# Kernel tuning notes

Measured on AMD Instinct MI355X. Metric: run time of the kernel, lower is better.

The kernel has to match this reference:

```python
import jax, jax.numpy as jnp
import numpy as np

H, D, K = 8, 64, 9           # new num heads, head size, conv kernel size
A = H * D                    # all_head_size = 512
HID = 2 * A                  # input hidden size = 1024
STD = 0.02


def setup_inputs() -> dict:
    key = jax.random.key(0)
    ks = jax.random.split(key, 16)
    B, S = 4, 2048
    f = jnp.float32
    inp = {
        'hidden_states': jax.random.normal(ks[0], (B, S, HID), f),
        'Wq': jax.random.normal(ks[1], (A, A), f) * STD,
        'bq': jnp.zeros((A,), f),
        'Wk': jax.random.normal(ks[2], (A, A), f) * STD,
        'bk': jnp.zeros((A,), f),
        'Wv': jax.random.normal(ks[3], (A, A), f) * STD,
        'bv': jnp.zeros((A,), f),
        'dw_w': jax.random.normal(ks[4], (A, 1, K), f) * STD,   # depthwise conv (groups=A)
        'pw_w': jax.random.normal(ks[5], (A, A, 1), f) * STD,   # pointwise 1x1 conv
        'sep_b': jnp.zeros((A, 1), f),                          # SeparableConv1D bias
        'Wck': jax.random.normal(ks[6], (H * K, A), f) * STD,   # conv_kernel_layer
        'bck': jnp.zeros((H * K,), f),
        'Wco': jax.random.normal(ks[7], (A, A), f) * STD,       # conv_out_layer
        'bco': jnp.zeros((A,), f),
    }
    return inp


def reference(hidden_states, Wq, bq, Wk, bk, Wv, bv, dw_w, pw_w, sep_b, Wck, bck, Wco, bco):
    B, S, _ = hidden_states.shape
    hs_attn = hidden_states[:, :, :A]
    hs_conv = hidden_states[:, :, A:]

    q = hs_attn @ Wq.T + bq
    k = hs_attn @ Wk.T + bk
    v = hs_attn @ Wv.T + bv

    # SeparableConv1D on (B, A, S): depthwise then pointwise, plus bias
    x = hs_conv.transpose(0, 2, 1)
    x = jax.lax.conv_general_dilated(
        x, dw_w, window_strides=(1,), padding=[(K // 2, K // 2)],
        feature_group_count=A, dimension_numbers=('NCH', 'OIH', 'NCH'))
    x = jnp.einsum('bcs,oc->bos', x, pw_w[:, :, 0]) + sep_b
    mixed_key_conv = x.transpose(0, 2, 1)            # (B,S,A)

    # per-token softmax conv kernel
    conv_attn = mixed_key_conv * hs_conv
    ckl = (conv_attn @ Wck.T + bck).reshape(B, S, H, K)
    ckl = jax.nn.softmax(ckl, axis=-1)               # softmax over kernel taps

    # dynamic-span lightweight convolution (unfold -> batched matmul)
    col = hs_conv @ Wco.T + bco                      # (B,S,A)
    pad = jnp.pad(col, ((0, 0), (K // 2, K // 2), (0, 0)))
    windows = jnp.stack([pad[:, i:i + S] for i in range(K)], axis=-1)  # (B,S,A,K)
    windows = windows.reshape(B, S, H, D, K)
    conv_out = jnp.einsum('bshdk,bshk->bshd', windows, ckl)            # (B,S,H,D)

    # standard self-attention
    qh = q.reshape(B, S, H, D).transpose(0, 2, 1, 3)
    kh = k.reshape(B, S, H, D).transpose(0, 2, 1, 3)
    vh = v.reshape(B, S, H, D).transpose(0, 2, 1, 3)
    scale = jnp.asarray(1.0 / np.sqrt(D), q.dtype)
    scores = jnp.einsum('bhqd,bhkd->bhqk', qh, kh) * scale
    probs = jax.nn.softmax(scores, axis=-1)
    ctx = jnp.einsum('bhqk,bhkd->bqhd', probs, vh)   # (B,S,H,D)

    out = jnp.concatenate([ctx, conv_out], axis=2)   # (B,S,2H,D)
    return out.reshape(B, S, HID)
```

## Files before the change

### kernel.cpp

```cpp
#include <hip/hip_runtime.h>
#include <hip/hip_bf16.h>

#define NH   8
#define HD   64
#define KW   9
#define AD   512
#define HIDD 1024
#define BB   4
#define SS   2048
#define MTOK (BB*SS)
#define WSZ  262144

typedef __attribute__((ext_vector_type(8))) short short8;
typedef __attribute__((ext_vector_type(4))) float floatx4;
typedef __attribute__((ext_vector_type(16))) float floatx16;

__device__ __forceinline__ short f2bf(float f) {
    unsigned u = __float_as_uint(f);
    u = (u + 0x7FFFu + ((u >> 16) & 1u)) >> 16;
    return (short)u;
}
__device__ __forceinline__ float bf2f(short s) {
    return __uint_as_float(((unsigned)(unsigned short)s) << 16);
}
__device__ __forceinline__ float exp2_raw(float x) {
    return __builtin_amdgcn_exp2f(x);
}
__device__ __forceinline__ unsigned pkbf2(float a, float b) {
    unsigned d;
    asm("v_cvt_pk_bf16_f32 %0, %1, %2" : "=v"(d) : "v"(a), "v"(b));
    return d;
}
__device__ __forceinline__ void gl2lds16(const short* g, short* l) {
    __builtin_amdgcn_global_load_lds(
        (const __attribute__((address_space(1))) void*)g,
        (__attribute__((address_space(3))) void*)l, 16, 0, 0);
}

__global__ __launch_bounds__(256) void cvt_hs_kernel(
    const float* __restrict__ hs, short* __restrict__ hsb)
{
    int idx = blockIdx.x * 256 + threadIdx.x;
    const float* s = hs + (long)idx * 8;
    float4 a = *(const float4*)s, c = *(const float4*)(s + 4);
    short8 o;
    o[0]=f2bf(a.x); o[1]=f2bf(a.y); o[2]=f2bf(a.z); o[3]=f2bf(a.w);
    o[4]=f2bf(c.x); o[5]=f2bf(c.y); o[6]=f2bf(c.z); o[7]=f2bf(c.w);
    *(short8*)(hsb + (long)idx * 8) = o;
}

__global__ __launch_bounds__(256) void cvt_w_kernel(
    const float* __restrict__ pw, const float* __restrict__ Wco,
    const float* __restrict__ Wq, const float* __restrict__ Wk,
    const float* __restrict__ Wv, const float* __restrict__ Wck,
    const float* __restrict__ dw,
    short* __restrict__ dst, float* __restrict__ dwT)
{
    int idx = blockIdx.x * 256 + threadIdx.x;
    if (idx >= 172032) {
        int t = idx - 172032;
        if (t < AD * KW) {
            int c = t / KW, k = t - c * KW;
            dwT[k * AD + c] = dw[t];
        }
        return;
    }
    int e0 = idx * 8;
    short8 o;
    if (e0 < 5 * WSZ) {
        int w = e0 >> 18, off = e0 & (WSZ - 1);
        const float* src = (w == 0) ? pw : (w == 1) ? Wco : (w == 2) ? Wq
                         : (w == 3) ? Wk : Wv;
        float4 a = *(const float4*)(src + off), c = *(const float4*)(src + off + 4);
        o[0]=f2bf(a.x); o[1]=f2bf(a.y); o[2]=f2bf(a.z); o[3]=f2bf(a.w);
        o[4]=f2bf(c.x); o[5]=f2bf(c.y); o[6]=f2bf(c.z); o[7]=f2bf(c.w);
    } else {
        int off = e0 - 5 * WSZ;
        int row = off >> 9, col = off & 511;
        if (row < NH * KW) {
            const float* src = Wck + row * AD + col;
            float4 a = *(const float4*)src, c = *(const float4*)(src + 4);
            o[0]=f2bf(a.x); o[1]=f2bf(a.y); o[2]=f2bf(a.z); o[3]=f2bf(a.w);
            o[4]=f2bf(c.x); o[5]=f2bf(c.y); o[6]=f2bf(c.z); o[7]=f2bf(c.w);
        } else {
            for (int i = 0; i < 8; ++i) o[i] = 0;
        }
    }
    *(short8*)(dst + e0) = o;
}

__global__ __launch_bounds__(256) void dwconv_kernel(
    const short* __restrict__ hsb, const float* __restrict__ dwT,
    short* __restrict__ x1)
{
    int idx = blockIdx.x * 256 + threadIdx.x;
    int c8  = (idx & 63) * 8;
    int tok = idx >> 6;
    int s   = tok & (SS - 1);
    int b   = tok >> 11;
    const short* base = hsb + (long)(b * SS) * HIDD + AD + c8;
    float acc[8];
#pragma unroll
    for (int i = 0; i < 8; ++i) acc[i] = 0.f;
#pragma unroll
    for (int kk = 0; kk < KW; ++kk) {
        int ss2 = s + kk - KW / 2;
        if (ss2 >= 0 && ss2 < SS) {
            short8 hv = *(const short8*)(base + (long)ss2 * HIDD);
            float4 w0 = *(const float4*)(dwT + kk * AD + c8);
            float4 w1 = *(const float4*)(dwT + kk * AD + c8 + 4);
            acc[0] += w0.x * bf2f(hv[0]); acc[1] += w0.y * bf2f(hv[1]);
            acc[2] += w0.z * bf2f(hv[2]); acc[3] += w0.w * bf2f(hv[3]);
            acc[4] += w1.x * bf2f(hv[4]); acc[5] += w1.y * bf2f(hv[5]);
            acc[6] += w1.z * bf2f(hv[6]); acc[7] += w1.w * bf2f(hv[7]);
        }
    }
    short8 o;
#pragma unroll
    for (int i = 0; i < 8; ++i) o[i] = f2bf(acc[i]);
    *(short8*)(x1 + (long)tok * AD + c8) = o;
}

template<int FM, int FN, int MODE>
__global__ __launch_bounds__(256) void gemm_bf16_kernel(
    const short* __restrict__ X, int ldx, int xoff,
    const short* __restrict__ W,
    const float* __restrict__ b0p, const float* __restrict__ b1p,
    const float* __restrict__ b2p,
    const short* __restrict__ mulp, int mul_ld, int mul_off,
    void* __restrict__ Cout, short* __restrict__ vtout,
    int ldc, int N, int Kd, float oscale)
{
    constexpr int TM = 32 * FM, TN = 32 * FN;
    __shared__ __align__(16) short As[TM * 64];
    __shared__ __align__(16) short Bs[TN * 64];
    const int tid  = threadIdx.x;
    const int wv   = tid >> 6, lane = tid & 63;
    const int ln   = lane & 15, quad = lane >> 4;
    const int wm   = wv >> 1, wn = wv & 1;
    const int m0 = blockIdx.x * TM, n0 = blockIdx.y * TN;

    floatx4 acc[FM][FN];
#pragma unroll
    for (int i = 0; i < FM; ++i)
#pragma unroll
        for (int j = 0; j < FN; ++j) acc[i][j] = (floatx4){0.f, 0.f, 0.f, 0.f};

    const short* xbase = X + (long)m0 * ldx + xoff;
    const short* wbase = W + (long)n0 * Kd;

    for (int k0 = 0; k0 < Kd; k0 += 64) {
#pragma unroll
        for (int g = tid; g < TM * 8; g += 256) {
            int m = g >> 3, p = g & 7, gk = p ^ (m & 7);
            gl2lds16(xbase + (long)m * ldx + k0 + gk * 8, &As[g * 8]);
        }
#pragma unroll
        for (int g = tid; g < TN * 8; g += 256) {
            int m = g >> 3, p = g & 7, gk = p ^ (m & 7);
            gl2lds16(wbase + (long)m * Kd + k0 + gk * 8, &Bs[g * 8]);
        }
        __syncthreads();
#pragma unroll
        for (int half = 0; half < 2; ++half) {
            short8 afr[FM], bfr[FN];
#pragma unroll
            for (int i = 0; i < FM; ++i) {
                int p = (half * 4 + quad) ^ (ln & 7);
                afr[i] = *(const short8*)&As[(wm * 16 * FM + i * 16 + ln) * 64 + p * 8];
            }
#pragma unroll
            for (int j = 0; j < FN; ++j) {
                int p = (half * 4 + quad) ^ (ln & 7);
                bfr[j] = *(const short8*)&Bs[(wn * 16 * FN + j * 16 + ln) * 64 + p * 8];
            }
#pragma unroll
            for (int i = 0; i < FM; ++i)
#pragma unroll
                for (int j = 0; j < FN; ++j)
                    acc[i][j] = __builtin_amdgcn_mfma_f32_16x16x32_bf16(
                        afr[i], bfr[j], acc[i][j], 0, 0, 0);
        }
        __syncthreads();
    }

#pragma unroll
    for (int j = 0; j < FN; ++j) {
        int n = n0 + wn * 16 * FN + j * 16 + ln;
        if constexpr (MODE == 3) {
            if (n >= 1024) {
                int hh = (n - 1024) >> 6, dd = (n - 1024) & 63;
                float bv = b2p[n - 1024];
                int mblk = m0 + wm * 16 * FM;
                int bidx = mblk >> 11, sblk = mblk & (SS - 1);
                short* dst = vtout + ((long)((bidx * NH + hh) * HD + dd)) * SS + sblk;
#pragma unroll
                for (int i = 0; i < FM; ++i) {
                    unsigned lo = pkbf2(acc[i][j][0] + bv, acc[i][j][1] + bv);
                    unsigned hi = pkbf2(acc[i][j][2] + bv, acc[i][j][3] + bv);
                    *(uint2*)(dst + i * 16 + quad * 4) = make_uint2(lo, hi);
                }
            } else {
                float bv = (n < 512) ? b0p[n] : b1p[n - 512];
                float sc = (n < 512) ? oscale : 1.f;
#pragma unroll
                for (int i = 0; i < FM; ++i) {
#pragma unroll
                    for (int r = 0; r < 4; ++r) {
                        int m = m0 + wm * 16 * FM + i * 16 + quad * 4 + r;
                        float val = (acc[i][j][r] + bv) * sc;
                        ((short*)Cout)[(long)m * ldc + n] = f2bf(val);
                    }
                }
            }
        } else if (n < N) {
            float bv = b0p[n], sc = oscale;
#pragma unroll
            for (int i = 0; i < FM; ++i) {
#pragma unroll
                for (int r = 0; r < 4; ++r) {
                    int m = m0 + wm * 16 * FM + i * 16 + quad * 4 + r;
                    float val = (acc[i][j][r] + bv) * sc;
                    if constexpr (MODE == 2)
                        val *= bf2f(mulp[(long)m * mul_ld + mul_off + n]);
                    if constexpr (MODE == 0)
                        ((float*)Cout)[(long)m * ldc + n] = val;
                    else
                        ((short*)Cout)[(long)m * ldc + n] = f2bf(val);
                }
            }
        }
    }
}

__global__ __launch_bounds__(256) void convout_kernel(
    const short* __restrict__ col, const float* __restrict__ ckl,
    float* __restrict__ out)
{
    int idx = blockIdx.x * 256 + threadIdx.x;
    int d4  = (idx & 127) * 4;
    int tok = idx >> 7;
    int s   = tok & (SS - 1);
    int b   = tok >> 11;
    int h   = d4 >> 6;
    const float* lg = ckl + (long)tok * (NH * KW) + h * KW;
    float wv[KW];
    float mx = -1e30f;
#pragma unroll
    for (int i = 0; i < KW; ++i) { wv[i] = lg[i]; mx = fmaxf(mx, wv[i]); }
    float sum = 0.f;
#pragma unroll
    for (int i = 0; i < KW; ++i) { wv[i] = __expf(wv[i] - mx); sum += wv[i]; }
    float inv = 1.f / sum;
    float a0 = 0.f, a1 = 0.f, a2 = 0.f, a3 = 0.f;
    const short* cbase = col + (long)(b * SS) * AD + d4;
#pragma unroll
    for (int kk = 0; kk < KW; ++kk) {
        int ss2 = s + kk - KW / 2;
        if (ss2 >= 0 && ss2 < SS) {
            uint2 cv = *(const uint2*)(cbase + (long)ss2 * AD);
            float w = wv[kk];
            a0 += w * bf2f((short)(cv.x & 0xFFFF));
            a1 += w * bf2f((short)(cv.x >> 16));
            a2 += w * bf2f((short)(cv.y & 0xFFFF));
            a3 += w * bf2f((short)(cv.y >> 16));
        }
    }
    *(float4*)&out[(long)tok * HIDD + AD + d4] =
        make_float4(a0 * inv, a1 * inv, a2 * inv, a3 * inv);
}

__global__ __launch_bounds__(256) void flash_mfma_kernel(
    const short* __restrict__ qkv, const short* __restrict__ vT,
    float* __restrict__ out)
{
    const int qt = blockIdx.x, h = blockIdx.y, b = blockIdx.z;
    const int tid  = threadIdx.x;
    const int w    = tid >> 6;
    const int lane = tid & 63;
    const int l5   = lane & 31;
    const int hh   = lane >> 5;

    __shared__ __align__(16) short Kb[3][4096];
    __shared__ __align__(16) short Vb[3][4096];
    __shared__ float ls[4][32];

    const int  q0 = qt * 128 + w * 32;
    const long rowbase = (long)b * SS;

    short8 qf[4];
    {
        const short* qrow = qkv + (rowbase + q0 + l5) * 1536 + h * HD;
#pragma unroll
        for (int i = 0; i < 4; ++i)
            qf[i] = *(const short8*)(qrow + i * 16 + hh * 8);
    }

    floatx16 acc0, acc1;
    floatx16 Z;
#pragma unroll
    for (int r = 0; r < 16; ++r) { acc0[r] = 0.f; acc1[r] = 0.f; Z[r] = 0.f; }
    float l_i = 0.f;

    const int m1 = tid >> 3,  gk1 = (tid & 7) ^ (m1 & 7);
    const int g2 = 256 + tid;
    const int m2 = g2 >> 3,   gk2 = (g2 & 7) ^ (m2 & 7);
    const short* kbase  = qkv + 512 + rowbase * 1536 + h * HD;
    const short* vtbase = vT + ((long)(b * NH + h) * HD) * SS;
    const short* sk0 = kbase  + (long)m1 * 1536 + gk1 * 8;
    const short* sk1 = kbase  + (long)m2 * 1536 + gk2 * 8;
    const short* sv0 = vtbase + (long)m1 * SS   + gk1 * 8;
    const short* sv1 = vtbase + (long)m2 * SS   + gk2 * 8;

    auto STAGE_K = [&](int slot, bool adv) {
        gl2lds16(sk0, &Kb[slot][tid * 8]);
        gl2lds16(sk1, &Kb[slot][g2 * 8]);
        if (adv) { sk0 += 64 * 1536; sk1 += 64 * 1536; }
    };
    auto STAGE_V = [&](int slot) {
        gl2lds16(sv0, &Vb[slot][tid * 8]);
        gl2lds16(sv1, &Vb[slot][g2 * 8]);
        sv0 += 64; sv1 += 64;
    };

    auto qkt = [&](const short* KB, floatx16& S0, floatx16& S1) {
        {
            int p = hh ^ (l5 & 7);
            short8 k0 = *(const short8*)&KB[l5 * 64 + p * 8];
            short8 k1 = *(const short8*)&KB[(32 + l5) * 64 + p * 8];
            S0 = __builtin_amdgcn_mfma_f32_32x32x16_bf16(k0, qf[0], Z, 0, 0, 0);
            S1 = __builtin_amdgcn_mfma_f32_32x32x16_bf16(k1, qf[0], Z, 0, 0, 0);
        }
#pragma unroll
        for (int i = 1; i < 4; ++i) {
            int p = (2 * i + hh) ^ (l5 & 7);
            short8 k0 = *(const short8*)&KB[l5 * 64 + p * 8];
            short8 k1 = *(const short8*)&KB[(32 + l5) * 64 + p * 8];
            S0 = __builtin_amdgcn_mfma_f32_32x32x16_bf16(k0, qf[i], S0, 0, 0, 0);
            S1 = __builtin_amdgcn_mfma_f32_32x32x16_bf16(k1, qf[i], S1, 0, 0, 0);
        }
    };

    auto smax = [&](const floatx16& S0, const floatx16& S1, short8* pf) {
        float pe0[16], pe1[16];
#pragma unroll
        for (int r = 0; r < 16; ++r) {
            pe0[r] = exp2_raw(S0[r]);
            pe1[r] = exp2_raw(S1[r]);
        }
        float s = 0.f;
#pragma unroll
        for (int r = 0; r < 16; ++r) s += pe0[r] + pe1[r];
        l_i += s;
#pragma unroll
        for (int t = 0; t < 2; ++t) {
            const float* pe = t ? pe1 : pe0;
#pragma unroll
            for (int u = 0; u < 2; ++u) {
                unsigned a0 = pkbf2(pe[8 * u + 0], pe[8 * u + 1]);
                unsigned a1 = pkbf2(pe[8 * u + 2], pe[8 * u + 3]);
                unsigned b0 = pkbf2(pe[8 * u + 4], pe[8 * u + 5]);
                unsigned b1 = pkbf2(pe[8 * u + 6], pe[8 * u + 7]);
                asm("v_permlane32_swap_b32 %0, %1" : "+v"(a0), "+v"(b0));
                asm("v_permlane32_swap_b32 %0, %1" : "+v"(a1), "+v"(b1));
                union { uint4 u4; short8 s8; } cv;
                cv.u4 = make_uint4(a0, a1, b0, b1);
                pf[t * 2 + u] = cv.s8;
            }
        }
    };

    auto pv = [&](const short* VB, const short8* pf) {
#pragma unroll
        for (int s = 0; s < 4; ++s) {
            int p = (2 * s + hh) ^ (l5 & 7);
            short8 v0 = *(const short8*)&VB[l5 * 64 + p * 8];
            short8 v1 = *(const short8*)&VB[(32 + l5) * 64 + p * 8];
            acc0 = __builtin_amdgcn_mfma_f32_32x32x16_bf16(pf[s], v0, acc0, 0, 0, 0);
            acc1 = __builtin_amdgcn_mfma_f32_32x32x16_bf16(pf[s], v1, acc1, 0, 0, 0);
        }
    };

    short8 pfA[4], pfB[4];

    STAGE_K(0, true);
    STAGE_K(1, true);
    STAGE_V(0);
    asm volatile("s_waitcnt vmcnt(0)" ::: "memory");
    __builtin_amdgcn_s_barrier();
    asm volatile("" ::: "memory");

    {
        STAGE_K(2, true);
        STAGE_V(1);
        floatx16 S0, S1;
        qkt(Kb[0], S0, S1);
        smax(S0, S1, pfA);
        asm volatile("s_waitcnt vmcnt(4)" ::: "memory");
        __builtin_amdgcn_s_barrier();
        asm volatile("" ::: "memory");
    }

#define PHASE(KS, VPS, KST, VST, KADV, PIN, POUT)                      \
    {                                                                  \
        STAGE_K(KST, KADV);                                            \
        STAGE_V(VST);                                                  \
        floatx16 S0, S1;                                               \
        __builtin_amdgcn_s_setprio(1);                                 \
        qkt(Kb[KS], S0, S1);                                           \
        pv(Vb[VPS], PIN);                                              \
        __builtin_amdgcn_s_setprio(0);                                 \
        smax(S0, S1, POUT);                                            \
        asm volatile("s_waitcnt vmcnt(4)" ::: "memory");               \
        __builtin_amdgcn_s_barrier();                                  \
        asm volatile("" ::: "memory");                                 \
    }

    for (int g = 0; g < 5; ++g) {
        bool notlast = (g < 4);
        PHASE(1, 0, 0, 2, true,    pfA, pfB);
        PHASE(2, 1, 1, 0, true,    pfB, pfA);
        PHASE(0, 2, 2, 1, true,    pfA, pfB);
        PHASE(1, 0, 0, 2, true,    pfB, pfA);
        PHASE(2, 1, 1, 0, notlast, pfA, pfB);
        PHASE(0, 2, 2, 1, notlast, pfB, pfA);
    }
#undef PHASE

    {
        floatx16 S0, S1;
        __builtin_amdgcn_s_setprio(1);
        qkt(Kb[1], S0, S1);
        pv(Vb[0], pfA);
        __builtin_amdgcn_s_setprio(0);
        smax(S0, S1, pfB);
        asm volatile("s_waitcnt vmcnt(0)" ::: "memory");
        __builtin_amdgcn_s_barrier();
        asm volatile("" ::: "memory");
    }
    pv(Vb[1], pfB);

    l_i += __shfl_xor(l_i, 32);
    ls[w][l5] = 1.f / l_i;
    float4 lv[4];
#pragma unroll
    for (int g = 0; g < 4; ++g)
        lv[g] = *(const float4*)&ls[w][8 * g + 4 * hh];

#pragma unroll
    for (int r = 0; r < 16; ++r) {
        int g = r >> 2, j = r & 3;
        int qr = j + 8 * g + 4 * hh;
        float iv = lv[g][j];
        float* orow = out + (rowbase + q0 + qr) * HIDD + h * HD;
        orow[l5]      = acc0[r] * iv;
        orow[32 + l5] = acc1[r] * iv;
    }
}

extern "C" void kernel_launch(void* const* d_in, const int* in_sizes, int n_in,
                              void* d_out, int out_size, void* d_ws, size_t ws_size,
                              hipStream_t stream)
{
    const float* hs   = (const float*)d_in[0];
    const float* Wq   = (const float*)d_in[1];
    const float* bq   = (const float*)d_in[2];
    const float* Wk   = (const float*)d_in[3];
    const float* bk   = (const float*)d_in[4];
    const float* Wv   = (const float*)d_in[5];
    const float* bv   = (const float*)d_in[6];
    const float* dw   = (const float*)d_in[7];
    const float* pw   = (const float*)d_in[8];
    const float* sepb = (const float*)d_in[9];
    const float* Wck  = (const float*)d_in[10];
    const float* bck  = (const float*)d_in[11];
    const float* Wco  = (const float*)d_in[12];
    const float* bco  = (const float*)d_in[13];
    float* out = (float*)d_out;

    short* hsb  = (short*)d_ws;
    short* x1c  = hsb + (long)MTOK * HIDD;
    short* qkvb = x1c + (long)MTOK * AD;
    short* vTb  = qkvb + (long)MTOK * 1536;
    float* ckl  = (float*)(vTb + (long)MTOK * AD);
    short* wb   = (short*)(ckl + (long)MTOK * (NH * KW));
    short* pw_b   = wb;
    short* Wco_b  = wb + 1L * WSZ;
    short* Wqkv_b = wb + 2L * WSZ;
    short* Wck_b  = wb + 5L * WSZ;
    float* dwT    = (float*)(Wck_b + 128L * AD);
    short* cab    = qkvb;

    const float QSCALE = 0.18033688011112042f;

    cvt_hs_kernel<<<MTOK * HIDD / 2048, 256, 0, stream>>>(hs, hsb);
    cvt_w_kernel<<<690, 256, 0, stream>>>(
        pw, Wco, Wq, Wk, Wv, Wck, dw, wb, dwT);
    dwconv_kernel<<<MTOK * AD / 2048, 256, 0, stream>>>(hsb, dwT, x1c);
    gemm_bf16_kernel<2, 2, 2><<<dim3(MTOK / 64, AD / 64), 256, 0, stream>>>(
        x1c, AD, 0, pw_b, sepb, nullptr, nullptr, hsb, HIDD, AD,
        cab, nullptr, AD, AD, AD, 1.f);
    gemm_bf16_kernel<2, 2, 0><<<dim3(MTOK / 64, 2), 256, 0, stream>>>(
        cab, AD, 0, Wck_b, bck, nullptr, nullptr, nullptr, 0, 0,
        ckl, nullptr, NH * KW, NH * KW, AD, 1.f);
    gemm_bf16_kernel<2, 2, 1><<<dim3(MTOK / 64, AD / 64), 256, 0, stream>>>(
        hsb, HIDD, AD, Wco_b, bco, nullptr, nullptr, nullptr, 0, 0,
        x1c, nullptr, AD, AD, AD, 1.f);
    convout_kernel<<<MTOK * AD / 1024, 256, 0, stream>>>(x1c, ckl, out);
    gemm_bf16_kernel<4, 4, 3><<<dim3(MTOK / 128, 1536 / 128), 256, 0, stream>>>(
        hsb, HIDD, 0, Wqkv_b, bq, bk, bv, nullptr, 0, 0,
        qkvb, vTb, 1536, 1536, AD, QSCALE);
    flash_mfma_kernel<<<dim3(SS / 128, NH, BB), 256, 0, stream>>>(qkvb, vTb, out);

    (void)in_sizes; (void)n_in; (void)out_size; (void)ws_size;
}
```

Before: 220.1 us.

## Merge prep and independent GEMMs into fewer horizontally fused launches

Combines the hidden-state conversion, weight conversion and depthwise conv into one prep kernel. The depthwise conv now reads fp32 input directly and keeps its weights in LDS, so it no longer waits on the bf16 copy. The QKV GEMM and the pointwise GEMM now share one launch, and the Wco and Wck GEMMs share a second, using larger tiles. This is meant to cut launch overhead and fill the GPU better. The conv-attention intermediate is now staged in the output buffer, which relies on convout and flash overwriting it later. Every prep block also allocates 18KB of LDS, which may limit occupancy for the simple convert blocks.

```diff
diff --git a/kernel.cpp b/kernel.cpp
--- a/kernel.cpp
+++ b/kernel.cpp
@@ -37,92 +37,89 @@
         (__attribute__((address_space(3))) void*)l, 16, 0, 0);
 }
 
-__global__ __launch_bounds__(256) void cvt_hs_kernel(
-    const float* __restrict__ hs, short* __restrict__ hsb)
-{
-    int idx = blockIdx.x * 256 + threadIdx.x;
-    const float* s = hs + (long)idx * 8;
-    float4 a = *(const float4*)s, c = *(const float4*)(s + 4);
-    short8 o;
-    o[0]=f2bf(a.x); o[1]=f2bf(a.y); o[2]=f2bf(a.z); o[3]=f2bf(a.w);
-    o[4]=f2bf(c.x); o[5]=f2bf(c.y); o[6]=f2bf(c.z); o[7]=f2bf(c.w);
-    *(short8*)(hsb + (long)idx * 8) = o;
-}
-
-__global__ __launch_bounds__(256) void cvt_w_kernel(
+__global__ __launch_bounds__(256) void prep_kernel(
+    const float* __restrict__ hs,
     const float* __restrict__ pw, const float* __restrict__ Wco,
     const float* __restrict__ Wq, const float* __restrict__ Wk,
     const float* __restrict__ Wv, const float* __restrict__ Wck,
     const float* __restrict__ dw,
-    short* __restrict__ dst, float* __restrict__ dwT)
-{
-    int idx = blockIdx.x * 256 + threadIdx.x;
-    if (idx >= 172032) {
-        int t = idx - 172032;
-        if (t < AD * KW) {
-            int c = t / KW, k = t - c * KW;
-            dwT[k * AD + c] = dw[t];
-        }
-        return;
-    }
-    int e0 = idx * 8;
-    short8 o;
-    if (e0 < 5 * WSZ) {
-        int w = e0 >> 18, off = e0 & (WSZ - 1);
-        const float* src = (w == 0) ? pw : (w == 1) ? Wco : (w == 2) ? Wq
-                         : (w == 3) ? Wk : Wv;
-        float4 a = *(const float4*)(src + off), c = *(const float4*)(src + off + 4);
+    short* __restrict__ hsb, short* __restrict__ wb, short* __restrict__ x1)
+{
+    __shared__ float wl[KW * AD];
+    const int bid = blockIdx.x, tid = threadIdx.x;
+
+    if (bid < 4096) {
+        int idx = bid * 256 + tid;
+        const float* s = hs + (long)idx * 8;
+        float4 a = *(const float4*)s, c = *(const float4*)(s + 4);
+        short8 o;
         o[0]=f2bf(a.x); o[1]=f2bf(a.y); o[2]=f2bf(a.z); o[3]=f2bf(a.w);
         o[4]=f2bf(c.x); o[5]=f2bf(c.y); o[6]=f2bf(c.z); o[7]=f2bf(c.w);
-    } else {
-        int off = e0 - 5 * WSZ;
-        int row = off >> 9, col = off & 511;
-        if (row < NH * KW) {
-            const float* src = Wck + row * AD + col;
-            float4 a = *(const float4*)src, c = *(const float4*)(src + 4);
+        *(short8*)(hsb + (long)idx * 8) = o;
+    } else if (bid < 4768) {
+        int idx = (bid - 4096) * 256 + tid;
+        int e0 = idx * 8;
+        short8 o;
+        if (e0 < 5 * WSZ) {
+            int w = e0 >> 18, off = e0 & (WSZ - 1);
+            const float* src = (w == 0) ? pw : (w == 1) ? Wco : (w == 2) ? Wq
+                             : (w == 3) ? Wk : Wv;
+            float4 a = *(const float4*)(src + off), c = *(const float4*)(src + off + 4);
             o[0]=f2bf(a.x); o[1]=f2bf(a.y); o[2]=f2bf(a.z); o[3]=f2bf(a.w);
             o[4]=f2bf(c.x); o[5]=f2bf(c.y); o[6]=f2bf(c.z); o[7]=f2bf(c.w);
         } else {
-            for (int i = 0; i < 8; ++i) o[i] = 0;
-        }
-    }
-    *(short8*)(dst + e0) = o;
-}
-
-__global__ __launch_bounds__(256) void dwconv_kernel(
-    const short* __restrict__ hsb, const float* __restrict__ dwT,
-    short* __restrict__ x1)
-{
-    int idx = blockIdx.x * 256 + threadIdx.x;
-    int c8  = (idx & 63) * 8;
-    int tok = idx >> 6;
-    int s   = tok & (SS - 1);
-    int b   = tok >> 11;
-    const short* base = hsb + (long)(b * SS) * HIDD + AD + c8;
-    float acc[8];
-#pragma unroll
-    for (int i = 0; i < 8; ++i) acc[i] = 0.f;
-#pragma unroll
-    for (int kk = 0; kk < KW; ++kk) {
-        int ss2 = s + kk - KW / 2;
-        if (ss2 >= 0 && ss2 < SS) {
-            short8 hv = *(const short8*)(base + (long)ss2 * HIDD);
-            float4 w0 = *(const float4*)(dwT + kk * AD + c8);
-            float4 w1 = *(const float4*)(dwT + kk * AD + c8 + 4);
-            acc[0] += w0.x * bf2f(hv[0]); acc[1] += w0.y * bf2f(hv[1]);
-            acc[2] += w0.z * bf2f(hv[2]); acc[3] += w0.w * bf2f(hv[3]);
-            acc[4] += w1.x * bf2f(hv[4]); acc[5] += w1.y * bf2f(hv[5]);
-            acc[6] += w1.z * bf2f(hv[6]); acc[7] += w1.w * bf2f(hv[7]);
-        }
-    }
-    short8 o;
-#pragma unroll
-    for (int i = 0; i < 8; ++i) o[i] = f2bf(acc[i]);
-    *(short8*)(x1 + (long)tok * AD + c8) = o;
+            int off = e0 - 5 * WSZ;
+            int row = off >> 9, col = off & 511;
+            if (row < NH * KW) {
+                const float* src = Wck + row * AD + col;
+                float4 a = *(const float4*)src, c = *(const float4*)(src + 4);
+                o[0]=f2bf(a.x); o[1]=f2bf(a.y); o[2]=f2bf(a.z); o[3]=f2bf(a.w);
+                o[4]=f2bf(c.x); o[5]=f2bf(c.y); o[6]=f2bf(c.z); o[7]=f2bf(c.w);
+            } else {
+                for (int i = 0; i < 8; ++i) o[i] = 0;
+            }
+        }
+        *(short8*)(wb + e0) = o;
+    } else {
+        for (int t = tid; t < KW * AD; t += 256) {
+            int c = t / KW, k = t - c * KW;
+            wl[k * AD + c] = dw[t];
+        }
+        __syncthreads();
+        int idx = (bid - 4768) * 256 + tid;
+        int c8  = (idx & 63) * 8;
+        int tok = idx >> 6;
+        int s   = tok & (SS - 1);
+        int b   = tok >> 11;
+        const float* base = hs + (long)(b * SS) * HIDD + AD + c8;
+        float acc[8];
+#pragma unroll
+        for (int i = 0; i < 8; ++i) acc[i] = 0.f;
+#pragma unroll
+        for (int kk = 0; kk < KW; ++kk) {
+            int ss2 = s + kk - KW / 2;
+            if (ss2 >= 0 && ss2 < SS) {
+                const float* hp = base + (long)ss2 * HIDD;
+                float4 h0 = *(const float4*)hp;
+                float4 h1 = *(const float4*)(hp + 4);
+                float4 w0 = *(const float4*)(wl + kk * AD + c8);
+                float4 w1 = *(const float4*)(wl + kk * AD + c8 + 4);
+                acc[0] += w0.x * h0.x; acc[1] += w0.y * h0.y;
+                acc[2] += w0.z * h0.z; acc[3] += w0.w * h0.w;
+                acc[4] += w1.x * h1.x; acc[5] += w1.y * h1.y;
+                acc[6] += w1.z * h1.z; acc[7] += w1.w * h1.w;
+            }
+        }
+        short8 o;
+#pragma unroll
+        for (int i = 0; i < 8; ++i) o[i] = f2bf(acc[i]);
+        *(short8*)(x1 + (long)tok * AD + c8) = o;
+    }
 }
 
 template<int FM, int FN, int MODE>
-__global__ __launch_bounds__(256) void gemm_bf16_kernel(
+__device__ __forceinline__ void gemm_body(
+    int bx, int by, short* As, short* Bs,
     const short* __restrict__ X, int ldx, int xoff,
     const short* __restrict__ W,
     const float* __restrict__ b0p, const float* __restrict__ b1p,
@@ -132,13 +129,11 @@
     int ldc, int N, int Kd, float oscale)
 {
     constexpr int TM = 32 * FM, TN = 32 * FN;
-    __shared__ __align__(16) short As[TM * 64];
-    __shared__ __align__(16) short Bs[TN * 64];
     const int tid  = threadIdx.x;
     const int wv   = tid >> 6, lane = tid & 63;
     const int ln   = lane & 15, quad = lane >> 4;
     const int wm   = wv >> 1, wn = wv & 1;
-    const int m0 = blockIdx.x * TM, n0 = blockIdx.y * TN;
+    const int m0 = bx * TM, n0 = by * TN;
 
     floatx4 acc[FM][FN];
 #pragma unroll
@@ -230,6 +225,50 @@
                 }
             }
         }
+    }
+}
+
+__global__ __launch_bounds__(256) void mega1_kernel(
+    const short* __restrict__ hsb, const short* __restrict__ x1c,
+    const short* __restrict__ Wqkv_b, const short* __restrict__ pw_b,
+    const float* __restrict__ bq, const float* __restrict__ bk,
+    const float* __restrict__ bv, const float* __restrict__ sepb,
+    short* __restrict__ qkvb, short* __restrict__ vTb,
+    short* __restrict__ cabO, float oscale)
+{
+    __shared__ __align__(16) short As[128 * 64];
+    __shared__ __align__(16) short Bs[128 * 64];
+    int bid = blockIdx.x;
+    if (bid < 768) {
+        gemm_body<4, 4, 3>(bid & 63, bid >> 6, As, Bs,
+            hsb, HIDD, 0, Wqkv_b, bq, bk, bv, nullptr, 0, 0,
+            qkvb, vTb, 1536, 1536, AD, oscale);
+    } else {
+        int id = bid - 768;
+        gemm_body<4, 2, 2>(id & 63, id >> 6, As, Bs,
+            x1c, AD, 0, pw_b, sepb, nullptr, nullptr, hsb, HIDD, AD,
+            cabO, nullptr, AD, AD, AD, 1.f);
+    }
+}
+
+__global__ __launch_bounds__(256) void mega2_kernel(
+    const short* __restrict__ hsb, const short* __restrict__ cabO,
+    const short* __restrict__ Wco_b, const short* __restrict__ Wck_b,
+    const float* __restrict__ bco, const float* __restrict__ bck,
+    short* __restrict__ x1c, float* __restrict__ ckl)
+{
+    __shared__ __align__(16) short As[128 * 64];
+    __shared__ __align__(16) short Bs[128 * 64];
+    int bid = blockIdx.x;
+    if (bid < 512) {
+        gemm_body<4, 2, 1>(bid & 63, bid >> 6, As, Bs,
+            hsb, HIDD, AD, Wco_b, bco, nullptr, nullptr, nullptr, 0, 0,
+            x1c, nullptr, AD, AD, AD, 1.f);
+    } else {
+        int id = bid - 512;
+        gemm_body<2, 2, 0>(id & 127, id >> 7, As, Bs,
+            cabO, AD, 0, Wck_b, bck, nullptr, nullptr, nullptr, 0, 0,
+            ckl, nullptr, NH * KW, NH * KW, AD, 1.f);
     }
 }
 
@@ -488,28 +527,17 @@
     short* Wco_b  = wb + 1L * WSZ;
     short* Wqkv_b = wb + 2L * WSZ;
     short* Wck_b  = wb + 5L * WSZ;
-    float* dwT    = (float*)(Wck_b + 128L * AD);
-    short* cab    = qkvb;
+    short* cabO   = (short*)d_out;
 
     const float QSCALE = 0.18033688011112042f;
 
-    cvt_hs_kernel<<<MTOK * HIDD / 2048, 256, 0, stream>>>(hs, hsb);
-    cvt_w_kernel<<<690, 256, 0, stream>>>(
-        pw, Wco, Wq, Wk, Wv, Wck, dw, wb, dwT);
-    dwconv_kernel<<<MTOK * AD / 2048, 256, 0, stream>>>(hsb, dwT, x1c);
-    gemm_bf16_kernel<2, 2, 2><<<dim3(MTOK / 64, AD / 64), 256, 0, stream>>>(
-        x1c, AD, 0, pw_b, sepb, nullptr, nullptr, hsb, HIDD, AD,
-        cab, nullptr, AD, AD, AD, 1.f);
-    gemm_bf16_kernel<2, 2, 0><<<dim3(MTOK / 64, 2), 256, 0, stream>>>(
-        cab, AD, 0, Wck_b, bck, nullptr, nullptr, nullptr, 0, 0,
-        ckl, nullptr, NH * KW, NH * KW, AD, 1.f);
-    gemm_bf16_kernel<2, 2, 1><<<dim3(MTOK / 64, AD / 64), 256, 0, stream>>>(
-        hsb, HIDD, AD, Wco_b, bco, nullptr, nullptr, nullptr, 0, 0,
-        x1c, nullptr, AD, AD, AD, 1.f);
+    prep_kernel<<<6816, 256, 0, stream>>>(
+        hs, pw, Wco, Wq, Wk, Wv, Wck, dw, hsb, wb, x1c);
+    mega1_kernel<<<1280, 256, 0, stream>>>(
+        hsb, x1c, Wqkv_b, pw_b, bq, bk, bv, sepb, qkvb, vTb, cabO, QSCALE);
+    mega2_kernel<<<768, 256, 0, stream>>>(
+        hsb, cabO, Wco_b, Wck_b, bco, bck, x1c, ckl);
     convout_kernel<<<MTOK * AD / 1024, 256, 0, stream>>>(x1c, ckl, out);
-    gemm_bf16_kernel<4, 4, 3><<<dim3(MTOK / 128, 1536 / 128), 256, 0, stream>>>(
-        hsb, HIDD, 0, Wqkv_b, bq, bk, bv, nullptr, 0, 0,
-        qkvb, vTb, 1536, 1536, AD, QSCALE);
     flash_mfma_kernel<<<dim3(SS / 128, NH, BB), 256, 0, stream>>>(qkvb, vTb, out);
 
     (void)in_sizes; (void)n_in; (void)out_size; (void)ws_size;
```

Measured after the change: 212.6 us. -3.4%, faster.
